# Performance work log

Measured on AMD Instinct MI355X. Metric: run time of the kernel, lower is better.

Reference implementation:

```python
import jax, jax.numpy as jnp
import numpy as np
from jax import lax

EPS = 1e-5
D_CONV = 4
D_STATE = 8

def layer_norm(x, g, b):
    mu = x.mean(-1, keepdims=True)
    var = x.var(-1, keepdims=True)
    return (x - mu) * lax.rsqrt(var + EPS) * g + b

def causal_dw_conv(x, w, b):
    # x: [B, D, L], w: [D, K] depthwise causal conv, b: [D]
    K = w.shape[1]
    xp = jnp.pad(x, ((0, 0), (0, 0), (K - 1, 0)))
    out = lax.conv_general_dilated(
        xp, w[:, None, :], window_strides=(1,), padding='VALID',
        dimension_numbers=('NCH', 'OIH', 'NCH'), feature_group_count=w.shape[0])
    return out + b[None, :, None]

def mamba(x, in_w, conv_w, conv_b, xp_w, dt_w, dt_b, A_log, D, out_w):
    # x: [B, L, d_model]; faithful to mamba_ssm Mamba forward (selective_scan_ref math)
    Bb, L, _ = x.shape
    d_inner = in_w.shape[0] // 2
    dt_rank = dt_w.shape[1]
    xz = jnp.einsum('bld,ed->ble', x, in_w)
    xi, z = jnp.split(xz, 2, axis=-1)                      # [B,L,d_inner] each
    xc = causal_dw_conv(xi.swapaxes(1, 2), conv_w, conv_b).swapaxes(1, 2)
    xc = jax.nn.silu(xc)                                   # [B,L,d_inner]
    dbl = jnp.einsum('bld,ed->ble', xc, xp_w)
    dt, Bs, Cs = jnp.split(dbl, [dt_rank, dt_rank + D_STATE], axis=-1)
    delta = jax.nn.softplus(jnp.einsum('blr,dr->bld', dt, dt_w) + dt_b)
    A = -jnp.exp(A_log)                                    # [d_inner, d_state]
    dA = jnp.exp(delta[..., None] * A)                     # [B,L,D,S]
    dBx = delta[..., None] * Bs[:, :, None, :] * xc[..., None]
    def step(h, inp):
        dA_t, dBx_t, c_t = inp
        h = dA_t * h + dBx_t                               # [B,D,S]
        return h, jnp.einsum('bds,bs->bd', h, c_t)
    h0 = jnp.zeros((Bb, d_inner, D_STATE), x.dtype)
    _, ys = lax.scan(step, h0, (dA.swapaxes(0, 1), dBx.swapaxes(0, 1), Cs.swapaxes(0, 1)))
    y = ys.swapaxes(0, 1) + xc * D                         # [B,L,D]
    y = y * jax.nn.silu(z)
    return jnp.einsum('bld,od->blo', y, out_w)

def setup_inputs() -> dict:
    key = jax.random.key(0)
    ks = jax.random.split(key, 4)
    B, C, H = 2, 128, 16
    L = H * H * H
    def nrm(k, shape, s=0.02):
        return jax.random.normal(k, shape, jnp.float32) * s
    inp = {}
    inp['x'] = jax.random.normal(ks[0], (B, C, H, H, H), jnp.float32)
    inp['ln1_g'] = jnp.ones((C,), jnp.float32)
    inp['ln1_b'] = jnp.zeros((C,), jnp.float32)
    inp['ln2_g'] = jnp.ones((L,), jnp.float32)
    inp['ln2_b'] = jnp.zeros((L,), jnp.float32)
    def mamba_params(kbase, d_model):
        d_inner = 2 * d_model
        dt_rank = d_model // 16
        kk = jax.random.split(kbase, 6)
        return {
            'in_w': nrm(kk[0], (2 * d_inner, d_model)),
            'conv_w': nrm(kk[1], (d_inner, D_CONV), 0.3),
            'conv_b': jnp.zeros((d_inner,), jnp.float32),
            'xp_w': nrm(kk[2], (dt_rank + 2 * D_STATE, d_inner)),
            'dt_w': nrm(kk[3], (d_inner, dt_rank), 0.1),
            'dt_b': jax.random.uniform(kk[4], (d_inner,), jnp.float32, -4.6, -2.3),
            'Alog': jnp.broadcast_to(jnp.log(jnp.arange(1, D_STATE + 1, dtype=jnp.float32)), (d_inner, D_STATE)) + jnp.zeros((d_inner, D_STATE), jnp.float32),
            'D': jnp.ones((d_inner,), jnp.float32),
            'out_w': nrm(kk[5], (d_model, d_inner)),
        }
    for pfx, dm, k in (('m1_', C, ks[1]), ('m2_', L, ks[2])):
        for name, v in mamba_params(k, dm).items():
            inp[pfx + name] = v
    return inp

def reference(x, ln1_g, ln1_b, ln2_g, ln2_b,
              m1_in_w, m1_conv_w, m1_conv_b, m1_xp_w, m1_dt_w, m1_dt_b, m1_Alog, m1_D, m1_out_w,
              m2_in_w, m2_conv_w, m2_conv_b, m2_xp_w, m2_dt_w, m2_dt_b, m2_Alog, m2_D, m2_out_w):
    B, C = x.shape[:2]
    xf = x.reshape(B, C, -1)          # [B, n_tokens, L]
    xc = xf.swapaxes(1, 2)            # [B, L, n_tokens]
    yc = mamba(layer_norm(xc, ln1_g, ln1_b),
               m1_in_w, m1_conv_w, m1_conv_b, m1_xp_w, m1_dt_w, m1_dt_b,
               m1_Alog, m1_D, m1_out_w).swapaxes(1, 2)
    ys = mamba(layer_norm(xf, ln2_g, ln2_b),
               m2_in_w, m2_conv_w, m2_conv_b, m2_xp_w, m2_dt_w, m2_dt_b,
               m2_Alog, m2_D, m2_out_w)
    # dropout is identity in eval mode
    return (yc + ys + xf).reshape(x.shape)
```

## Files before the change

kernel.cpp:

```cpp
#include <hip/hip_runtime.h>
#include <math.h>

typedef __attribute__((ext_vector_type(8))) short s16x8;
typedef __attribute__((ext_vector_type(4))) short s16x4;
typedef __attribute__((ext_vector_type(4))) float f32x4;

#define DEVINL __device__ __forceinline__

DEVINL short f2bf(float f) {
    unsigned u = __float_as_uint(f);
    u += 0x7fffu + ((u >> 16) & 1u);
    return (short)(u >> 16);
}
DEVINL float softplusf(float x) { return (x > 20.f) ? x : log1pf(expf(x)); }
DEVINL float siluf(float z) { return z / (1.f + expf(-z)); }

__global__ __launch_bounds__(256) void ln1_kernel(const float* __restrict__ x,
    const float* __restrict__ g, const float* __restrict__ bb, short* __restrict__ out)
{
    __shared__ float tile[64 * 129];
    int b = blockIdx.x >> 6;
    int l0 = (blockIdx.x & 63) << 6;
    int t = threadIdx.x;
    int ll = t & 63, c0 = t >> 6;
    for (int c = c0; c < 128; c += 4)
        tile[ll * 129 + c] = x[((size_t)(b * 128 + c) << 12) + l0 + ll];
    __syncthreads();
    int r = t >> 2, q = t & 3;
    float s1 = 0.f, s2 = 0.f;
    #pragma unroll 8
    for (int j = 0; j < 32; ++j) {
        float v = tile[r * 129 + q * 32 + j];
        s1 += v; s2 += v * v;
    }
    s1 += __shfl_xor(s1, 1); s2 += __shfl_xor(s2, 1);
    s1 += __shfl_xor(s1, 2); s2 += __shfl_xor(s2, 2);
    float mean = s1 * (1.f / 128.f);
    float var  = s2 * (1.f / 128.f) - mean * mean;
    float rstd = rsqrtf(var + 1e-5f);
    short* orow = out + ((size_t)((b << 12) + l0 + r) << 7);
    for (int j = 0; j < 32; j += 4) {
        int c = q * 32 + j;
        s16x4 pk;
        #pragma unroll
        for (int i = 0; i < 4; ++i)
            pk[i] = f2bf((tile[r * 129 + c + i] - mean) * rstd * g[c + i] + bb[c + i]);
        *(s16x4*)&orow[c] = pk;
    }
}

__global__ __launch_bounds__(256) void ln2_kernel(const float* __restrict__ x,
    const float* __restrict__ g, const float* __restrict__ bb, short* __restrict__ out)
{
    int m = blockIdx.x, t = threadIdx.x;
    const float* row = x + (size_t)m * 4096;
    f32x4 vals[4];
    float s1 = 0.f, s2 = 0.f;
    #pragma unroll
    for (int j = 0; j < 4; ++j) {
        vals[j] = *(const f32x4*)(row + j * 1024 + t * 4);
        #pragma unroll
        for (int i = 0; i < 4; ++i) { s1 += vals[j][i]; s2 += vals[j][i] * vals[j][i]; }
    }
    #pragma unroll
    for (int off = 32; off; off >>= 1) { s1 += __shfl_xor(s1, off); s2 += __shfl_xor(s2, off); }
    __shared__ float red[8];
    int wv = t >> 6;
    if ((t & 63) == 0) { red[wv] = s1; red[4 + wv] = s2; }
    __syncthreads();
    s1 = red[0] + red[1] + red[2] + red[3];
    s2 = red[4] + red[5] + red[6] + red[7];
    float mean = s1 * (1.f / 4096.f);
    float var  = s2 * (1.f / 4096.f) - mean * mean;
    float rstd = rsqrtf(var + 1e-5f);
    short* orow = out + (size_t)m * 4096;
    #pragma unroll
    for (int j = 0; j < 4; ++j) {
        int idx = j * 1024 + t * 4;
        f32x4 gv = *(const f32x4*)(g + idx);
        f32x4 bv = *(const f32x4*)(bb + idx);
        s16x4 pk;
        #pragma unroll
        for (int i = 0; i < 4; ++i)
            pk[i] = f2bf((vals[j][i] - mean) * rstd * gv[i] + bv[i]);
        *(s16x4*)&orow[idx] = pk;
    }
}

template<int BM, int BN, int EPI>
__global__ __launch_bounds__(256) void gemm_bt(
    const short* __restrict__ A, const float* __restrict__ W,
    float* __restrict__ C, const float* __restrict__ bias,
    int M, int Nreal, int K, int kLen, int ldc)
{
    constexpr int LK = 72;
    __shared__ short Al[BM * LK];
    __shared__ short Wl[BN * LK];
    const int tid = threadIdx.x;
    const int lane = tid & 63;
    const int wv = tid >> 6;
    const int lr = lane & 15, kh = lane >> 4;
    const int n0 = blockIdx.x * BN;
    const int m0 = blockIdx.y * BM;
    const int k0 = blockIdx.z * kLen;
    constexpr int FM = BM / 64, FN = BN / 16;
    f32x4 acc[FM][FN];
    #pragma unroll
    for (int a = 0; a < FM; ++a)
        #pragma unroll
        for (int b = 0; b < FN; ++b) acc[a][b] = (f32x4){0.f, 0.f, 0.f, 0.f};

    for (int kt = 0; kt < kLen; kt += 64) {
        const int kg = k0 + kt;
        {
            int ar = tid >> 3, ac = tid & 7;
            #pragma unroll
            for (int i = 0; i < BM / 32; ++i) {
                int row = ar + i * 32;
                s16x8 v = *(const s16x8*)(A + (size_t)(m0 + row) * K + kg + ac * 8);
                *(s16x8*)&Al[row * LK + ac * 8] = v;
            }
        }
        {
            #pragma unroll
            for (int j = 0; j < (BN * 16) / 256; ++j) {
                int chunk = tid + j * 256;
                int row = chunk >> 4, cc = chunk & 15;
                int gn = n0 + row;
                f32x4 v;
                if (gn < Nreal) v = *(const f32x4*)(W + (size_t)gn * K + kg + cc * 4);
                else            v = (f32x4){0.f, 0.f, 0.f, 0.f};
                s16x4 pk;
                #pragma unroll
                for (int i = 0; i < 4; ++i) pk[i] = f2bf(v[i]);
                *(s16x4*)&Wl[row * LK + cc * 4] = pk;
            }
        }
        __syncthreads();
        #pragma unroll
        for (int ks = 0; ks < 64; ks += 32) {
            s16x8 af[FM], bfr[FN];
            #pragma unroll
            for (int mi = 0; mi < FM; ++mi)
                af[mi] = *(const s16x8*)&Al[(wv * (BM / 4) + mi * 16 + lr) * LK + ks + kh * 8];
            #pragma unroll
            for (int ni = 0; ni < FN; ++ni)
                bfr[ni] = *(const s16x8*)&Wl[(ni * 16 + lr) * LK + ks + kh * 8];
            #pragma unroll
            for (int mi = 0; mi < FM; ++mi)
                #pragma unroll
                for (int ni = 0; ni < FN; ++ni)
                    acc[mi][ni] = __builtin_amdgcn_mfma_f32_16x16x32_bf16(
                        af[mi], bfr[ni], acc[mi][ni], 0, 0, 0);
        }
        __syncthreads();
    }
    float* Cz = C + (size_t)blockIdx.z * M * ldc;
    #pragma unroll
    for (int mi = 0; mi < FM; ++mi) {
        #pragma unroll
        for (int ni = 0; ni < FN; ++ni) {
            int gn = n0 + ni * 16 + lr;
            #pragma unroll
            for (int j = 0; j < 4; ++j) {
                int gm = m0 + wv * (BM / 4) + mi * 16 + kh * 4 + j;
                float v = acc[mi][ni][j];
                if constexpr (EPI == 1) v = softplusf(v + bias[gn]);
                Cz[(size_t)gm * ldc + gn] = v;
            }
        }
    }
}

__global__ __launch_bounds__(256) void conv1_kernel(const float* __restrict__ xz,
    const float* __restrict__ cw, const float* __restrict__ cb,
    float* __restrict__ xcf, short* __restrict__ xcb)
{
    int idx = blockIdx.x * 256 + threadIdx.x;
    int d = idx & 255;
    int l = (idx >> 8) & 4095;
    int b = idx >> 20;
    f32x4 wv = *(const f32x4*)(cw + d * 4);
    float acc = cb[d];
    #pragma unroll
    for (int j = 0; j < 4; ++j) {
        int ll = l - 3 + j;
        if (ll >= 0) acc += xz[((size_t)((b << 12) + ll) << 9) + d] * wv[j];
    }
    acc = siluf(acc);
    size_t o = ((size_t)((b << 12) + l) << 8) + d;
    xcf[o] = acc;
    xcb[o] = f2bf(acc);
}

__global__ __launch_bounds__(256) void conv2_kernel(const float* __restrict__ xz,
    const float* __restrict__ cw, const float* __restrict__ cb,
    float* __restrict__ xcf, short* __restrict__ xcb)
{
    int idx = blockIdx.x * 256 + threadIdx.x;
    int d = idx & 8191;
    int t = (idx >> 13) & 127;
    int b = idx >> 20;
    f32x4 wv = *(const f32x4*)(cw + d * 4);
    float acc = cb[d];
    #pragma unroll
    for (int j = 0; j < 4; ++j) {
        int tt = t - 3 + j;
        if (tt >= 0) acc += xz[((size_t)((b << 7) + tt) << 14) + d] * wv[j];
    }
    acc = siluf(acc);
    size_t o = ((size_t)((b << 7) + t) << 13) + d;
    xcf[o] = acc;
    xcb[o] = f2bf(acc);
}

__global__ __launch_bounds__(256) void dtproj1_kernel(const float* __restrict__ dbl,
    const float* __restrict__ dtw, const float* __restrict__ dtb, float* __restrict__ delta)
{
    int m = blockIdx.x;
    int d = threadIdx.x;
    const float* dtv = dbl + (size_t)m * 32;
    f32x4 w0 = *(const f32x4*)(dtw + d * 8);
    f32x4 w1 = *(const f32x4*)(dtw + d * 8 + 4);
    float acc = dtb[d];
    #pragma unroll
    for (int j = 0; j < 4; ++j) acc += dtv[j] * w0[j];
    #pragma unroll
    for (int j = 0; j < 4; ++j) acc += dtv[4 + j] * w1[j];
    delta[(size_t)m * 256 + d] = softplusf(acc);
}

__global__ __launch_bounds__(256) void scan1_p1(const float* __restrict__ delta,
    const float* __restrict__ xc, const float* __restrict__ dbl,
    const float* __restrict__ alog, float* __restrict__ hch, float* __restrict__ pch)
{
    int b = blockIdx.x >> 6, ch = blockIdx.x & 63;
    int d = threadIdx.x;
    __shared__ float bc[1024];
    for (int i = threadIdx.x; i < 1024; i += 256) {
        int j = i >> 4, s = i & 15;
        bc[i] = dbl[(size_t)((b << 12) + (ch << 6) + j) * 32 + 8 + s];
    }
    float a[8], h[8], P[8];
    #pragma unroll
    for (int s = 0; s < 8; ++s) { a[s] = -expf(alog[d * 8 + s]); h[s] = 0.f; P[s] = 1.f; }
    __syncthreads();
    for (int j = 0; j < 64; ++j) {
        size_t row = (b << 12) + (ch << 6) + j;
        float dl = delta[(row << 8) + d];
        float xv = xc[(row << 8) + d];
        float dx = dl * xv;
        #pragma unroll
        for (int s = 0; s < 8; ++s) {
            float dA = expf(dl * a[s]);
            h[s] = dA * h[s] + dx * bc[(j << 4) + s];
            P[s] *= dA;
        }
    }
    size_t base = (((size_t)((b << 6) + ch) << 8) + d) << 3;
    #pragma unroll
    for (int s = 0; s < 8; ++s) { hch[base + s] = h[s]; pch[base + s] = P[s]; }
}

__global__ __launch_bounds__(256) void scan1_p2(const float* __restrict__ hch,
    const float* __restrict__ pch, float* __restrict__ hin)
{
    int b = blockIdx.x >> 3;
    int idx = ((blockIdx.x & 7) << 8) + threadIdx.x;
    float h = 0.f;
    for (int c = 0; c < 64; ++c) {
        size_t o = (((size_t)((b << 6) + c)) << 11) + idx;
        hin[o] = h;
        h = pch[o] * h + hch[o];
    }
}

__global__ __launch_bounds__(256) void scan1_p3(const float* __restrict__ delta,
    const float* __restrict__ xc, const float* __restrict__ dbl,
    const float* __restrict__ alog, const float* __restrict__ hin,
    const float* __restrict__ Dw, const float* __restrict__ xz,
    short* __restrict__ ybf)
{
    int b = blockIdx.x >> 6, ch = blockIdx.x & 63;
    int d = threadIdx.x;
    __shared__ float bc[1024];
    for (int i = threadIdx.x; i < 1024; i += 256) {
        int j = i >> 4, s = i & 15;
        bc[i] = dbl[(size_t)((b << 12) + (ch << 6) + j) * 32 + 8 + s];
    }
    float a[8], h[8];
    size_t base = (((size_t)((b << 6) + ch) << 8) + d) << 3;
    #pragma unroll
    for (int s = 0; s < 8; ++s) { a[s] = -expf(alog[d * 8 + s]); h[s] = hin[base + s]; }
    float Dv = Dw[d];
    __syncthreads();
    for (int j = 0; j < 64; ++j) {
        size_t row = (b << 12) + (ch << 6) + j;
        float dl = delta[(row << 8) + d];
        float xv = xc[(row << 8) + d];
        float dx = dl * xv;
        float y = 0.f;
        #pragma unroll
        for (int s = 0; s < 8; ++s) {
            float dA = expf(dl * a[s]);
            h[s] = dA * h[s] + dx * bc[(j << 4) + s];
            y += h[s] * bc[(j << 4) + 8 + s];
        }
        float z = xz[(row << 9) + 256 + d];
        ybf[(row << 8) + d] = f2bf((y + xv * Dv) * siluf(z));
    }
}

__global__ void xp2_finish(const float* __restrict__ part, short* __restrict__ dtb,
                           float* __restrict__ Bs, float* __restrict__ Cs)
{
    int m = blockIdx.x, t = threadIdx.x;
    if (t >= 272) return;
    float s = 0.f;
    #pragma unroll
    for (int p = 0; p < 16; ++p) s += part[(size_t)p * 73728 + m * 288 + t];
    if (t < 256)       dtb[m * 256 + t] = f2bf(s);
    else if (t < 264)  Bs[m * 8 + t - 256] = s;
    else               Cs[m * 8 + t - 264] = s;
}

__global__ __launch_bounds__(256) void scan2_kernel(const float* __restrict__ delta,
    const float* __restrict__ xc, const float* __restrict__ Bs,
    const float* __restrict__ Cs, const float* __restrict__ xz,
    const float* __restrict__ alog, const float* __restrict__ Dw,
    short* __restrict__ ybf)
{
    int b = blockIdx.x >> 5;
    int d = ((blockIdx.x & 31) << 8) + threadIdx.x;
    __shared__ float bc[2048];
    for (int i = threadIdx.x; i < 2048; i += 256) {
        int t = i >> 4, s = i & 15;
        bc[i] = (s < 8) ? Bs[((b << 7) + t) * 8 + s] : Cs[((b << 7) + t) * 8 + s - 8];
    }
    float a[8], h[8];
    #pragma unroll
    for (int s = 0; s < 8; ++s) { a[s] = -expf(alog[(size_t)d * 8 + s]); h[s] = 0.f; }
    float Dv = Dw[d];
    __syncthreads();
    for (int t = 0; t < 128; ++t) {
        size_t row = (b << 7) + t;
        float dl = delta[(row << 13) + d];
        float xv = xc[(row << 13) + d];
        float dx = dl * xv;
        float y = 0.f;
        #pragma unroll
        for (int s = 0; s < 8; ++s) {
            float dA = expf(dl * a[s]);
            h[s] = dA * h[s] + dx * bc[(t << 4) + s];
            y += h[s] * bc[(t << 4) + 8 + s];
        }
        float z = xz[(row << 14) + 8192 + d];
        ybf[(row << 13) + d] = f2bf((y + xv * Dv) * siluf(z));
    }
}

__global__ __launch_bounds__(256) void final_kernel(const float* __restrict__ x,
    const float* __restrict__ y1out, const float* __restrict__ part2,
    float* __restrict__ out)
{
    __shared__ float tl[64 * 65];
    int bz = blockIdx.x;
    int b = bz >> 7, rem = bz & 127;
    int c0 = (rem >> 6) << 6, l0 = (rem & 63) << 6;
    int t = threadIdx.x;
    int lrow = t >> 4, cq = (t & 15) << 2;
    #pragma unroll
    for (int jj = 0; jj < 4; ++jj) {
        int l = l0 + lrow + jj * 16;
        f32x4 v = *(const f32x4*)&y1out[((size_t)((b << 12) + l) << 7) + c0 + cq];
        #pragma unroll
        for (int i = 0; i < 4; ++i) tl[(cq + i) * 65 + lrow + jj * 16] = v[i];
    }
    __syncthreads();
    int lc = t & 63, cr = t >> 6;
    for (int j = 0; j < 16; ++j) {
        int cl = j * 4 + cr;
        size_t addr = ((size_t)((b << 7) + c0 + cl) << 12) + l0 + lc;
        float v = x[addr] + tl[cl * 65 + lc];
        v += part2[addr] + part2[1048576 + addr] + part2[2 * 1048576 + addr] + part2[3 * 1048576 + addr];
        out[addr] = v;
    }
}

extern "C" void kernel_launch(void* const* d_in, const int* in_sizes, int n_in,
                              void* d_out, int out_size, void* d_ws, size_t ws_size,
                              hipStream_t stream)
{
    (void)in_sizes; (void)n_in; (void)out_size; (void)ws_size;
    const float* x        = (const float*)d_in[0];
    const float* ln1_g    = (const float*)d_in[1];
    const float* ln1_b    = (const float*)d_in[2];
    const float* ln2_g    = (const float*)d_in[3];
    const float* ln2_b    = (const float*)d_in[4];
    const float* m1_in_w  = (const float*)d_in[5];
    const float* m1_cw    = (const float*)d_in[6];
    const float* m1_cb    = (const float*)d_in[7];
    const float* m1_xp_w  = (const float*)d_in[8];
    const float* m1_dt_w  = (const float*)d_in[9];
    const float* m1_dt_b  = (const float*)d_in[10];
    const float* m1_Alog  = (const float*)d_in[11];
    const float* m1_D     = (const float*)d_in[12];
    const float* m1_out_w = (const float*)d_in[13];
    const float* m2_in_w  = (const float*)d_in[14];
    const float* m2_cw    = (const float*)d_in[15];
    const float* m2_cb    = (const float*)d_in[16];
    const float* m2_xp_w  = (const float*)d_in[17];
    const float* m2_dt_w  = (const float*)d_in[18];
    const float* m2_dt_b  = (const float*)d_in[19];
    const float* m2_Alog  = (const float*)d_in[20];
    const float* m2_D     = (const float*)d_in[21];
    const float* m2_out_w = (const float*)d_in[22];
    float* out = (float*)d_out;

    char* wsp = (char*)d_ws;
    size_t off = 0;
    auto alloc = [&](size_t bytes) -> void* {
        void* p = wsp + off;
        off += (bytes + 255) & ~(size_t)255;
        return p;
    };

    float* y1out = (float*)alloc((size_t)8192 * 128 * 4);
    size_t off0 = off;

    short* xln1   = (short*)alloc((size_t)8192 * 128 * 2);
    float* xz1    = (float*)alloc((size_t)8192 * 512 * 4);
    float* xc1f   = (float*)alloc((size_t)8192 * 256 * 4);
    short* xc1b   = (short*)alloc((size_t)8192 * 256 * 2);
    float* dbl1   = (float*)alloc((size_t)8192 * 32 * 4);
    float* delta1 = (float*)alloc((size_t)8192 * 256 * 4);
    float* hch    = (float*)alloc((size_t)128 * 2048 * 4);
    float* pch    = (float*)alloc((size_t)128 * 2048 * 4);
    float* hin    = (float*)alloc((size_t)128 * 2048 * 4);
    short* y1b    = (short*)alloc((size_t)8192 * 256 * 2);

    ln1_kernel<<<128, 256, 0, stream>>>(x, ln1_g, ln1_b, xln1);
    gemm_bt<256, 64, 0><<<dim3(8, 32, 1), 256, 0, stream>>>(xln1, m1_in_w, xz1, nullptr, 8192, 512, 128, 128, 512);
    conv1_kernel<<<8192, 256, 0, stream>>>(xz1, m1_cw, m1_cb, xc1f, xc1b);
    gemm_bt<128, 32, 0><<<dim3(1, 64, 1), 256, 0, stream>>>(xc1b, m1_xp_w, dbl1, nullptr, 8192, 24, 256, 256, 32);
    dtproj1_kernel<<<8192, 256, 0, stream>>>(dbl1, m1_dt_w, m1_dt_b, delta1);
    scan1_p1<<<128, 256, 0, stream>>>(delta1, xc1f, dbl1, m1_Alog, hch, pch);
    scan1_p2<<<16, 256, 0, stream>>>(hch, pch, hin);
    scan1_p3<<<128, 256, 0, stream>>>(delta1, xc1f, dbl1, m1_Alog, hin, m1_D, xz1, y1b);
    gemm_bt<128, 64, 0><<<dim3(2, 64, 1), 256, 0, stream>>>(y1b, m1_out_w, y1out, nullptr, 8192, 128, 256, 256, 128);

    off = off0;
    short* xln2   = (short*)alloc((size_t)256 * 4096 * 2);
    float* xz2    = (float*)alloc((size_t)256 * 16384 * 4);
    float* xc2f   = (float*)alloc((size_t)256 * 8192 * 4);
    short* xc2b   = (short*)alloc((size_t)256 * 8192 * 2);
    float* xp2p   = (float*)alloc((size_t)16 * 256 * 288 * 4);
    short* dt2b   = (short*)alloc((size_t)256 * 256 * 2);
    float* Bs2    = (float*)alloc((size_t)256 * 8 * 4);
    float* Cs2    = (float*)alloc((size_t)256 * 8 * 4);
    float* delta2 = (float*)alloc((size_t)256 * 8192 * 4);
    short* y2b    = (short*)alloc((size_t)256 * 8192 * 2);
    float* out2p  = (float*)alloc((size_t)4 * 256 * 4096 * 4);

    ln2_kernel<<<256, 256, 0, stream>>>(x, ln2_g, ln2_b, xln2);
    gemm_bt<256, 32, 0><<<dim3(512, 1, 1), 256, 0, stream>>>(xln2, m2_in_w, xz2, nullptr, 256, 16384, 4096, 4096, 16384);
    conv2_kernel<<<8192, 256, 0, stream>>>(xz2, m2_cw, m2_cb, xc2f, xc2b);
    gemm_bt<256, 32, 0><<<dim3(9, 1, 16), 256, 0, stream>>>(xc2b, m2_xp_w, xp2p, nullptr, 256, 272, 8192, 512, 288);
    xp2_finish<<<256, 288, 0, stream>>>(xp2p, dt2b, Bs2, Cs2);
    gemm_bt<256, 32, 1><<<dim3(256, 1, 1), 256, 0, stream>>>(dt2b, m2_dt_w, delta2, m2_dt_b, 256, 8192, 256, 256, 8192);
    scan2_kernel<<<64, 256, 0, stream>>>(delta2, xc2f, Bs2, Cs2, xz2, m2_Alog, m2_D, y2b);
    gemm_bt<256, 32, 0><<<dim3(128, 1, 4), 256, 0, stream>>>(y2b, m2_out_w, out2p, nullptr, 256, 4096, 8192, 2048, 4096);
    final_kernel<<<256, 256, 0, stream>>>(x, y1out, out2p, out);
}
```

Before: 919.3 us.

## Double-buffer GEMM with async LDS loads, swizzle, and widen scan parallelism

The GEMM now double-buffers LDS tiles, loads A straight into LDS with global_load_lds, and uses an XOR swizzle instead of padding. Its warp layout is configurable, and the tile shapes, grids and split-K factors of every GEMM launch are retuned. The scan kernels are split into more chunks, and scan2 launches more, smaller blocks, to raise occupancy on long sequential loops. Scan1_p2 prefetches the next chunk's values. Together these aim to hide global latency, but they add LDS use, more partials to reduce, and a longer sequential combine in scan1_p2.

```diff
diff --git a/kernel.cpp b/kernel.cpp
--- a/kernel.cpp
+++ b/kernel.cpp
@@ -14,6 +14,12 @@
 }
 DEVINL float softplusf(float x) { return (x > 20.f) ? x : log1pf(expf(x)); }
 DEVINL float siluf(float z) { return z / (1.f + expf(-z)); }
+
+typedef __attribute__((address_space(1))) const unsigned GblU32;
+typedef __attribute__((address_space(3))) unsigned LdsU32;
+DEVINL void gload_lds16(const void* g, void* l) {
+    __builtin_amdgcn_global_load_lds((GblU32*)g, (LdsU32*)l, 16, 0, 0);
+}
 
 __global__ __launch_bounds__(256) void ln1_kernel(const float* __restrict__ x,
     const float* __restrict__ g, const float* __restrict__ bb, short* __restrict__ out)
@@ -87,65 +93,83 @@
     }
 }
 
-template<int BM, int BN, int EPI>
+template<int BM, int BN, int WM, int WN, int EPI>
 __global__ __launch_bounds__(256) void gemm_bt(
     const short* __restrict__ A, const float* __restrict__ W,
     float* __restrict__ C, const float* __restrict__ bias,
     int M, int Nreal, int K, int kLen, int ldc)
 {
-    constexpr int LK = 72;
-    __shared__ short Al[BM * LK];
-    __shared__ short Wl[BN * LK];
+    constexpr int FM = BM / (WM * 16);
+    constexpr int FN = BN / (WN * 16);
+    constexpr int NISSA = BM / 32;
+    constexpr int NW = (BN * 16) / 256;
+    __shared__ short Al[2][BM * 64];
+    __shared__ short Wl[2][BN * 64];
     const int tid = threadIdx.x;
     const int lane = tid & 63;
     const int wv = tid >> 6;
     const int lr = lane & 15, kh = lane >> 4;
+    const int wm = wv % WM, wn = wv / WM;
     const int n0 = blockIdx.x * BN;
     const int m0 = blockIdx.y * BM;
     const int k0 = blockIdx.z * kLen;
-    constexpr int FM = BM / 64, FN = BN / 16;
+    const int nt = kLen >> 6;
+    const int srcSlot = (lane & 7) ^ (lane >> 3);
+
     f32x4 acc[FM][FN];
     #pragma unroll
     for (int a = 0; a < FM; ++a)
         #pragma unroll
         for (int b = 0; b < FN; ++b) acc[a][b] = (f32x4){0.f, 0.f, 0.f, 0.f};
-
-    for (int kt = 0; kt < kLen; kt += 64) {
-        const int kg = k0 + kt;
-        {
-            int ar = tid >> 3, ac = tid & 7;
+    f32x4 wreg[NW];
+
+    auto stageA = [&](int buf, int kg) {
+        #pragma unroll
+        for (int i = 0; i < NISSA; ++i) {
+            int c = wv * NISSA + i;
+            int r = c * 8 + (lane >> 3);
+            const short* src = A + (size_t)(m0 + r) * K + kg + srcSlot * 8;
+            gload_lds16(src, &Al[buf][c * 512]);
+        }
+    };
+    auto loadW = [&](int kg) {
+        #pragma unroll
+        for (int j = 0; j < NW; ++j) {
+            int idx = j * 256 + tid;
+            int row = idx >> 4, q = idx & 15;
+            int gn = n0 + row;
+            if (gn < Nreal) wreg[j] = *(const f32x4*)(W + (size_t)gn * K + kg + q * 4);
+            else            wreg[j] = (f32x4){0.f, 0.f, 0.f, 0.f};
+        }
+    };
+    auto writeW = [&](int buf) {
+        #pragma unroll
+        for (int j = 0; j < NW; ++j) {
+            int idx = j * 256 + tid;
+            int row = idx >> 4, q = idx & 15;
+            s16x4 pk;
             #pragma unroll
-            for (int i = 0; i < BM / 32; ++i) {
-                int row = ar + i * 32;
-                s16x8 v = *(const s16x8*)(A + (size_t)(m0 + row) * K + kg + ac * 8);
-                *(s16x8*)&Al[row * LK + ac * 8] = v;
-            }
-        }
-        {
-            #pragma unroll
-            for (int j = 0; j < (BN * 16) / 256; ++j) {
-                int chunk = tid + j * 256;
-                int row = chunk >> 4, cc = chunk & 15;
-                int gn = n0 + row;
-                f32x4 v;
-                if (gn < Nreal) v = *(const f32x4*)(W + (size_t)gn * K + kg + cc * 4);
-                else            v = (f32x4){0.f, 0.f, 0.f, 0.f};
-                s16x4 pk;
-                #pragma unroll
-                for (int i = 0; i < 4; ++i) pk[i] = f2bf(v[i]);
-                *(s16x4*)&Wl[row * LK + cc * 4] = pk;
-            }
-        }
-        __syncthreads();
-        #pragma unroll
-        for (int ks = 0; ks < 64; ks += 32) {
+            for (int i = 0; i < 4; ++i) pk[i] = f2bf(wreg[j][i]);
+            int byte = row * 128 + (((q >> 1) ^ (row & 7)) << 4) + ((q & 1) << 3);
+            *(s16x4*)((char*)&Wl[buf][0] + byte) = pk;
+        }
+    };
+    auto compute = [&](int buf) {
+        #pragma unroll
+        for (int ks = 0; ks < 2; ++ks) {
             s16x8 af[FM], bfr[FN];
             #pragma unroll
-            for (int mi = 0; mi < FM; ++mi)
-                af[mi] = *(const s16x8*)&Al[(wv * (BM / 4) + mi * 16 + lr) * LK + ks + kh * 8];
+            for (int mi = 0; mi < FM; ++mi) {
+                int r = wm * (BM / WM) + mi * 16 + lr;
+                int byte = r * 128 + (((ks * 4 + kh) ^ (r & 7)) << 4);
+                af[mi] = *(const s16x8*)((const char*)&Al[buf][0] + byte);
+            }
             #pragma unroll
-            for (int ni = 0; ni < FN; ++ni)
-                bfr[ni] = *(const s16x8*)&Wl[(ni * 16 + lr) * LK + ks + kh * 8];
+            for (int ni = 0; ni < FN; ++ni) {
+                int w = wn * (BN / WN) + ni * 16 + lr;
+                int byte = w * 128 + (((ks * 4 + kh) ^ (w & 7)) << 4);
+                bfr[ni] = *(const s16x8*)((const char*)&Wl[buf][0] + byte);
+            }
             #pragma unroll
             for (int mi = 0; mi < FM; ++mi)
                 #pragma unroll
@@ -153,20 +177,37 @@
                     acc[mi][ni] = __builtin_amdgcn_mfma_f32_16x16x32_bf16(
                         af[mi], bfr[ni], acc[mi][ni], 0, 0, 0);
         }
+    };
+
+    loadW(k0);
+    stageA(0, k0);
+    writeW(0);
+    __syncthreads();
+
+    int cur = 0;
+    for (int t = 0; t < nt; ++t) {
+        const int kn = k0 + (t + 1) * 64;
+        if (t + 1 < nt) { loadW(kn); stageA(cur ^ 1, kn); }
+        compute(cur);
+        if (t + 1 < nt) writeW(cur ^ 1);
         __syncthreads();
-    }
+        cur ^= 1;
+    }
+
     float* Cz = C + (size_t)blockIdx.z * M * ldc;
     #pragma unroll
     for (int mi = 0; mi < FM; ++mi) {
         #pragma unroll
         for (int ni = 0; ni < FN; ++ni) {
-            int gn = n0 + ni * 16 + lr;
-            #pragma unroll
-            for (int j = 0; j < 4; ++j) {
-                int gm = m0 + wv * (BM / 4) + mi * 16 + kh * 4 + j;
-                float v = acc[mi][ni][j];
-                if constexpr (EPI == 1) v = softplusf(v + bias[gn]);
-                Cz[(size_t)gm * ldc + gn] = v;
+            int gn = n0 + wn * (BN / WN) + ni * 16 + lr;
+            if (gn < Nreal) {
+                #pragma unroll
+                for (int j = 0; j < 4; ++j) {
+                    int gm = m0 + wm * (BM / WM) + mi * 16 + kh * 4 + j;
+                    float v = acc[mi][ni][j];
+                    if constexpr (EPI == 1) v = softplusf(v + bias[gn]);
+                    Cz[(size_t)gm * ldc + gn] = v;
+                }
             }
         }
     }
@@ -234,19 +275,19 @@
     const float* __restrict__ xc, const float* __restrict__ dbl,
     const float* __restrict__ alog, float* __restrict__ hch, float* __restrict__ pch)
 {
-    int b = blockIdx.x >> 6, ch = blockIdx.x & 63;
+    int b = blockIdx.x >> 7, ch = blockIdx.x & 127;
     int d = threadIdx.x;
-    __shared__ float bc[1024];
-    for (int i = threadIdx.x; i < 1024; i += 256) {
+    __shared__ float bc[512];
+    for (int i = threadIdx.x; i < 512; i += 256) {
         int j = i >> 4, s = i & 15;
-        bc[i] = dbl[(size_t)((b << 12) + (ch << 6) + j) * 32 + 8 + s];
+        bc[i] = dbl[(size_t)((b << 12) + (ch << 5) + j) * 32 + 8 + s];
     }
     float a[8], h[8], P[8];
     #pragma unroll
     for (int s = 0; s < 8; ++s) { a[s] = -expf(alog[d * 8 + s]); h[s] = 0.f; P[s] = 1.f; }
     __syncthreads();
-    for (int j = 0; j < 64; ++j) {
-        size_t row = (b << 12) + (ch << 6) + j;
+    for (int j = 0; j < 32; ++j) {
+        size_t row = (b << 12) + (ch << 5) + j;
         float dl = delta[(row << 8) + d];
         float xv = xc[(row << 8) + d];
         float dx = dl * xv;
@@ -257,7 +298,7 @@
             P[s] *= dA;
         }
     }
-    size_t base = (((size_t)((b << 6) + ch) << 8) + d) << 3;
+    size_t base = (((size_t)((b << 7) + ch) << 8) + d) << 3;
     #pragma unroll
     for (int s = 0; s < 8; ++s) { hch[base + s] = h[s]; pch[base + s] = P[s]; }
 }
@@ -268,10 +309,15 @@
     int b = blockIdx.x >> 3;
     int idx = ((blockIdx.x & 7) << 8) + threadIdx.x;
     float h = 0.f;
-    for (int c = 0; c < 64; ++c) {
-        size_t o = (((size_t)((b << 6) + c)) << 11) + idx;
+    size_t o0 = (((size_t)(b << 7)) << 11) + idx;
+    float pc = pch[o0], hc = hch[o0];
+    for (int c = 0; c < 128; ++c) {
+        size_t o = (((size_t)((b << 7) + c)) << 11) + idx;
+        float pn = 0.f, hn = 0.f;
+        if (c < 127) { pn = pch[o + 2048]; hn = hch[o + 2048]; }
         hin[o] = h;
-        h = pch[o] * h + hch[o];
+        h = pc * h + hc;
+        pc = pn; hc = hn;
     }
 }
 
@@ -281,21 +327,21 @@
     const float* __restrict__ Dw, const float* __restrict__ xz,
     short* __restrict__ ybf)
 {
-    int b = blockIdx.x >> 6, ch = blockIdx.x & 63;
+    int b = blockIdx.x >> 7, ch = blockIdx.x & 127;
     int d = threadIdx.x;
-    __shared__ float bc[1024];
-    for (int i = threadIdx.x; i < 1024; i += 256) {
+    __shared__ float bc[512];
+    for (int i = threadIdx.x; i < 512; i += 256) {
         int j = i >> 4, s = i & 15;
-        bc[i] = dbl[(size_t)((b << 12) + (ch << 6) + j) * 32 + 8 + s];
+        bc[i] = dbl[(size_t)((b << 12) + (ch << 5) + j) * 32 + 8 + s];
     }
     float a[8], h[8];
-    size_t base = (((size_t)((b << 6) + ch) << 8) + d) << 3;
+    size_t base = (((size_t)((b << 7) + ch) << 8) + d) << 3;
     #pragma unroll
     for (int s = 0; s < 8; ++s) { a[s] = -expf(alog[d * 8 + s]); h[s] = hin[base + s]; }
     float Dv = Dw[d];
     __syncthreads();
-    for (int j = 0; j < 64; ++j) {
-        size_t row = (b << 12) + (ch << 6) + j;
+    for (int j = 0; j < 32; ++j) {
+        size_t row = (b << 12) + (ch << 5) + j;
         float dl = delta[(row << 8) + d];
         float xv = xc[(row << 8) + d];
         float dx = dl * xv;
@@ -318,22 +364,22 @@
     if (t >= 272) return;
     float s = 0.f;
     #pragma unroll
-    for (int p = 0; p < 16; ++p) s += part[(size_t)p * 73728 + m * 288 + t];
+    for (int p = 0; p < 32; ++p) s += part[(size_t)p * 73728 + m * 288 + t];
     if (t < 256)       dtb[m * 256 + t] = f2bf(s);
     else if (t < 264)  Bs[m * 8 + t - 256] = s;
     else               Cs[m * 8 + t - 264] = s;
 }
 
-__global__ __launch_bounds__(256) void scan2_kernel(const float* __restrict__ delta,
+__global__ __launch_bounds__(64) void scan2_kernel(const float* __restrict__ delta,
     const float* __restrict__ xc, const float* __restrict__ Bs,
     const float* __restrict__ Cs, const float* __restrict__ xz,
     const float* __restrict__ alog, const float* __restrict__ Dw,
     short* __restrict__ ybf)
 {
-    int b = blockIdx.x >> 5;
-    int d = ((blockIdx.x & 31) << 8) + threadIdx.x;
+    int b = blockIdx.x >> 7;
+    int d = ((blockIdx.x & 127) << 6) + threadIdx.x;
     __shared__ float bc[2048];
-    for (int i = threadIdx.x; i < 2048; i += 256) {
+    for (int i = threadIdx.x; i < 2048; i += 64) {
         int t = i >> 4, s = i & 15;
         bc[i] = (s < 8) ? Bs[((b << 7) + t) * 8 + s] : Cs[((b << 7) + t) * 8 + s - 8];
     }
@@ -434,27 +480,27 @@
     short* xc1b   = (short*)alloc((size_t)8192 * 256 * 2);
     float* dbl1   = (float*)alloc((size_t)8192 * 32 * 4);
     float* delta1 = (float*)alloc((size_t)8192 * 256 * 4);
-    float* hch    = (float*)alloc((size_t)128 * 2048 * 4);
-    float* pch    = (float*)alloc((size_t)128 * 2048 * 4);
-    float* hin    = (float*)alloc((size_t)128 * 2048 * 4);
+    float* hch    = (float*)alloc((size_t)256 * 2048 * 4);
+    float* pch    = (float*)alloc((size_t)256 * 2048 * 4);
+    float* hin    = (float*)alloc((size_t)256 * 2048 * 4);
     short* y1b    = (short*)alloc((size_t)8192 * 256 * 2);
 
     ln1_kernel<<<128, 256, 0, stream>>>(x, ln1_g, ln1_b, xln1);
-    gemm_bt<256, 64, 0><<<dim3(8, 32, 1), 256, 0, stream>>>(xln1, m1_in_w, xz1, nullptr, 8192, 512, 128, 128, 512);
+    gemm_bt<128, 64, 2, 2, 0><<<dim3(8, 64, 1), 256, 0, stream>>>(xln1, m1_in_w, xz1, nullptr, 8192, 512, 128, 128, 512);
     conv1_kernel<<<8192, 256, 0, stream>>>(xz1, m1_cw, m1_cb, xc1f, xc1b);
-    gemm_bt<128, 32, 0><<<dim3(1, 64, 1), 256, 0, stream>>>(xc1b, m1_xp_w, dbl1, nullptr, 8192, 24, 256, 256, 32);
+    gemm_bt<128, 32, 2, 2, 0><<<dim3(1, 64, 1), 256, 0, stream>>>(xc1b, m1_xp_w, dbl1, nullptr, 8192, 24, 256, 256, 32);
     dtproj1_kernel<<<8192, 256, 0, stream>>>(dbl1, m1_dt_w, m1_dt_b, delta1);
-    scan1_p1<<<128, 256, 0, stream>>>(delta1, xc1f, dbl1, m1_Alog, hch, pch);
+    scan1_p1<<<256, 256, 0, stream>>>(delta1, xc1f, dbl1, m1_Alog, hch, pch);
     scan1_p2<<<16, 256, 0, stream>>>(hch, pch, hin);
-    scan1_p3<<<128, 256, 0, stream>>>(delta1, xc1f, dbl1, m1_Alog, hin, m1_D, xz1, y1b);
-    gemm_bt<128, 64, 0><<<dim3(2, 64, 1), 256, 0, stream>>>(y1b, m1_out_w, y1out, nullptr, 8192, 128, 256, 256, 128);
+    scan1_p3<<<256, 256, 0, stream>>>(delta1, xc1f, dbl1, m1_Alog, hin, m1_D, xz1, y1b);
+    gemm_bt<128, 64, 2, 2, 0><<<dim3(2, 64, 1), 256, 0, stream>>>(y1b, m1_out_w, y1out, nullptr, 8192, 128, 256, 256, 128);
 
     off = off0;
     short* xln2   = (short*)alloc((size_t)256 * 4096 * 2);
     float* xz2    = (float*)alloc((size_t)256 * 16384 * 4);
     float* xc2f   = (float*)alloc((size_t)256 * 8192 * 4);
     short* xc2b   = (short*)alloc((size_t)256 * 8192 * 2);
-    float* xp2p   = (float*)alloc((size_t)16 * 256 * 288 * 4);
+    float* xp2p   = (float*)alloc((size_t)32 * 256 * 288 * 4);
     short* dt2b   = (short*)alloc((size_t)256 * 256 * 2);
     float* Bs2    = (float*)alloc((size_t)256 * 8 * 4);
     float* Cs2    = (float*)alloc((size_t)256 * 8 * 4);
@@ -463,12 +509,12 @@
     float* out2p  = (float*)alloc((size_t)4 * 256 * 4096 * 4);
 
     ln2_kernel<<<256, 256, 0, stream>>>(x, ln2_g, ln2_b, xln2);
-    gemm_bt<256, 32, 0><<<dim3(512, 1, 1), 256, 0, stream>>>(xln2, m2_in_w, xz2, nullptr, 256, 16384, 4096, 4096, 16384);
+    gemm_bt<256, 64, 4, 1, 0><<<dim3(256, 1, 1), 256, 0, stream>>>(xln2, m2_in_w, xz2, nullptr, 256, 16384, 4096, 4096, 16384);
     conv2_kernel<<<8192, 256, 0, stream>>>(xz2, m2_cw, m2_cb, xc2f, xc2b);
-    gemm_bt<256, 32, 0><<<dim3(9, 1, 16), 256, 0, stream>>>(xc2b, m2_xp_w, xp2p, nullptr, 256, 272, 8192, 512, 288);
+    gemm_bt<256, 64, 4, 1, 0><<<dim3(5, 1, 32), 256, 0, stream>>>(xc2b, m2_xp_w, xp2p, nullptr, 256, 272, 8192, 256, 288);
     xp2_finish<<<256, 288, 0, stream>>>(xp2p, dt2b, Bs2, Cs2);
-    gemm_bt<256, 32, 1><<<dim3(256, 1, 1), 256, 0, stream>>>(dt2b, m2_dt_w, delta2, m2_dt_b, 256, 8192, 256, 256, 8192);
-    scan2_kernel<<<64, 256, 0, stream>>>(delta2, xc2f, Bs2, Cs2, xz2, m2_Alog, m2_D, y2b);
-    gemm_bt<256, 32, 0><<<dim3(128, 1, 4), 256, 0, stream>>>(y2b, m2_out_w, out2p, nullptr, 256, 4096, 8192, 2048, 4096);
+    gemm_bt<256, 64, 4, 1, 1><<<dim3(128, 1, 1), 256, 0, stream>>>(dt2b, m2_dt_w, delta2, m2_dt_b, 256, 8192, 256, 256, 8192);
+    scan2_kernel<<<256, 64, 0, stream>>>(delta2, xc2f, Bs2, Cs2, xz2, m2_Alog, m2_D, y2b);
+    gemm_bt<256, 64, 4, 1, 0><<<dim3(64, 1, 4), 256, 0, stream>>>(y2b, m2_out_w, out2p, nullptr, 256, 4096, 8192, 2048, 4096);
     final_kernel<<<256, 256, 0, stream>>>(x, y1out, out2p, out);
 }
```

New measurement: 831.9 us. 9.5% less time.
